# Kernel tuning notes

Measured on AMD Instinct MI355X. Metric: run time of the kernel, lower is better.

Reference implementation:

```python
import jax, jax.numpy as jnp
import numpy as np

NUM_CLASSES = 21
OVERLAP_THRESH = 0.5
POS_PRIOR_THRESH = 0.01
NEGPOS_RATIO = 3
ARM_VAR = (0.1, 0.2)
VAR = (0.1, 0.2)
B, P, NOBJ = 64, 16320, 32


def _iou(a, b):
    # a: [N,4] point-form, b: [P,4] point-form -> [N,P]
    lt = jnp.maximum(a[:, None, :2], b[None, :, :2])
    rb = jnp.minimum(a[:, None, 2:], b[None, :, 2:])
    wh = jnp.clip(rb - lt, 0.0)
    inter = wh[..., 0] * wh[..., 1]
    area_a = (a[:, 2] - a[:, 0]) * (a[:, 3] - a[:, 1])
    area_b = (b[:, 2] - b[:, 0]) * (b[:, 3] - b[:, 1])
    return inter / (area_a[:, None] + area_b[None, :] - inter)


def _decode_point(loc, priors, var):
    # loc: [P,4], priors: [P,4] center-form -> [P,4] point-form
    cxcy = priors[:, :2] + loc[:, :2] * var[0] * priors[:, 2:]
    wh = priors[:, 2:] * jnp.exp(loc[:, 2:] * var[1])
    return jnp.concatenate([cxcy - wh / 2, cxcy + wh / 2], axis=-1)


def _encode(matched, priors, var):
    # matched: [P,4] point-form gt, priors: [P,4] center-form -> [P,4]
    g_cxcy = ((matched[:, :2] + matched[:, 2:]) / 2 - priors[:, :2]) / (var[0] * priors[:, 2:])
    g_wh = jnp.log((matched[:, 2:] - matched[:, :2]) / priors[:, 2:]) / var[1]
    return jnp.concatenate([g_cxcy, g_wh], axis=-1)


def _match_one(truths, labels, dec_point, ref_center, reserve):
    # truths:[N,4] labels:[N] dec_point/ref_center:[P,4] reserve:[P] bool
    n_obj = truths.shape[0]
    ov = _iou(truths, dec_point)                       # [N,P]
    ovm = jnp.where(reserve[None, :], ov, -1.0)        # mask out filtered priors
    best_prior_idx = jnp.argmax(ovm, axis=1)           # [N]
    best_truth_overlap = jnp.max(ovm, axis=0)          # [P]
    best_truth_idx = jnp.argmax(ovm, axis=0)           # [P]
    best_truth_overlap = best_truth_overlap.at[best_prior_idx].set(2.0)
    best_truth_idx = best_truth_idx.at[best_prior_idx].set(jnp.arange(n_obj))
    matched = truths[best_truth_idx]                   # [P,4]
    conf = labels[best_truth_idx] + 1                  # [P]
    conf = jnp.where(best_truth_overlap < OVERLAP_THRESH, 0, conf)
    loc = _encode(matched, ref_center, VAR)
    conf = jnp.where(reserve, conf, -1)                # ignored priors
    loc = jnp.where(reserve[:, None], loc, 0.0)
    return loc, conf


def setup_inputs() -> dict:
    key = jax.random.key(0)
    ks = jax.random.split(key, 8)
    arm_loc = 0.1 * jax.random.normal(ks[0], (B, P, 4), dtype=jnp.float32)
    arm_conf = jax.random.normal(ks[1], (B, P, 2), dtype=jnp.float32)
    odm_loc = jax.random.normal(ks[2], (B, P, 4), dtype=jnp.float32)
    odm_conf = jax.random.normal(ks[3], (B, P, NUM_CLASSES), dtype=jnp.float32)
    # center-form anchors: valid cx,cy,w,h
    cxcy = jax.random.uniform(ks[4], (P, 2), minval=0.02, maxval=0.98)
    wh = jax.random.uniform(ks[5], (P, 2), minval=0.05, maxval=0.4)
    priors = jnp.concatenate([cxcy, wh], axis=-1).astype(jnp.float32)
    # valid point-form ground-truth boxes
    tc = jax.random.uniform(ks[6], (B, NOBJ, 2), minval=0.2, maxval=0.8)
    tw = jax.random.uniform(ks[7], (B, NOBJ, 2), minval=0.05, maxval=0.3)
    truths = jnp.concatenate([tc - tw / 2, tc + tw / 2], axis=-1).astype(jnp.float32)
    labels = jax.random.randint(jax.random.fold_in(key, 9), (B, NOBJ), 0, 20)
    return {"arm_loc": arm_loc, "arm_conf": arm_conf, "odm_loc": odm_loc,
            "odm_conf": odm_conf, "priors": priors, "truths": truths,
            "labels": labels}


def reference(arm_loc, arm_conf, odm_loc, odm_conf, priors, truths, labels):
    # ARM branch and targets are constants w.r.t. gradients (torch uses .data)
    arm_loc = jax.lax.stop_gradient(arm_loc)
    arm_conf = jax.lax.stop_gradient(arm_conf)
    truths = jax.lax.stop_gradient(truths)
    priors = jax.lax.stop_gradient(priors)

    arm_pos_prob = jax.nn.softmax(arm_conf, axis=-1)[..., 1]       # [B,P]
    reserve = arm_pos_prob > POS_PRIOR_THRESH                      # [B,P]
    dec_point = jax.vmap(lambda l: _decode_point(l, priors, ARM_VAR))(arm_loc)  # [B,P,4]
    ref_center = jnp.concatenate([(dec_point[..., :2] + dec_point[..., 2:]) / 2,
                                  dec_point[..., 2:] - dec_point[..., :2]], axis=-1)
    loc_t, conf_t = jax.vmap(_match_one)(truths, labels, dec_point, ref_center, reserve)
    loc_t = jax.lax.stop_gradient(loc_t)
    conf_t = jax.lax.stop_gradient(conf_t)

    pos = conf_t > 0                                               # [B,P]
    ignore = conf_t == -1
    conf_t0 = jnp.where(ignore, 0, conf_t)

    # localization: smooth L1 over positives (sum)
    d = jnp.abs(odm_loc - loc_t)
    sl1 = jnp.where(d < 1.0, 0.5 * d * d, d - 0.5)
    loss_l = jnp.sum(sl1 * pos[..., None].astype(sl1.dtype))

    # per-prior CE: logsumexp - target logit
    lse = jax.nn.logsumexp(odm_conf, axis=-1)                      # [B,P]
    tgt = jnp.take_along_axis(odm_conf, conf_t0[..., None], axis=-1)[..., 0]
    ce = lse - tgt                                                 # [B,P]

    # hard-negative mining: rank negatives by CE (double argsort)
    mine = jnp.where(pos | ignore, 0.0, ce)
    order = jnp.argsort(-mine, axis=1)
    rank = jnp.argsort(order, axis=1)
    num_pos = jnp.sum(pos, axis=1, keepdims=True)                  # [B,1]
    num_neg = jnp.minimum(NEGPOS_RATIO * num_pos, P - 1)
    neg = rank < num_neg

    loss_c = jnp.sum(jnp.where(pos | neg, ce, 0.0))
    total_num = jnp.sum(num_pos).astype(jnp.float32)
    return (loss_l / total_num, loss_c / total_num)
```

## Files before the change

### kernel.cpp

```cpp
#include <hip/hip_runtime.h>

#define B 64
#define P 16320
#define NOBJ 32
#define NC 21
#define CHUNK 4080

__device__ constexpr float LN99 = 4.59511985013459f;
#define SENT 0x407FFFFFFFFFFFFFULL

__global__ void k_init(int* num_pos, float* ll_b, float* lc_b) {
    int t = threadIdx.x;
    if (t < B) { num_pos[t] = 0; ll_b[t] = 0.f; lc_b[t] = 0.f; }
}

__global__ __launch_bounds__(1024) void k_p1(
    const float* __restrict__ arm_loc, const float* __restrict__ arm_conf,
    const float* __restrict__ priors, const float* __restrict__ truths,
    int* __restrict__ bt_pack, unsigned long long* __restrict__ bp_part)
{
    int b = blockIdx.x >> 2, c = blockIdx.x & 3;
    int tid = threadIdx.x;
    int base = c * CHUNK;

    __shared__ float4 s_tr[NOBJ];
    __shared__ float s_ta[NOBJ];
    __shared__ unsigned long long s1[NOBJ * 256];
    __shared__ unsigned long long s2[1024];

    if (tid < NOBJ) {
        float4 t = ((const float4*)truths)[b * NOBJ + tid];
        s_tr[tid] = t;
        s_ta[tid] = (t.z - t.x) * (t.w - t.y);
    }
    __syncthreads();

    float x1[4], y1[4], x2[4], y2[4], ap[4];
    bool rs[4], av[4];
    #pragma unroll
    for (int g = 0; g < 4; g++) {
        int off = g * 1024 + tid;
        av[g] = off < CHUNK;
        rs[g] = false;
        x1[g] = y1[g] = x2[g] = y2[g] = ap[g] = 0.f;
        if (av[g]) {
            int p = base + off;
            size_t bpi = (size_t)b * P + p;
            float2 cc = ((const float2*)arm_conf)[bpi];
            rs[g] = (cc.x - cc.y) < LN99;
            float4 l = ((const float4*)arm_loc)[bpi];
            float4 pr = ((const float4*)priors)[p];
            float dcx = pr.x + l.x * 0.1f * pr.z;
            float dcy = pr.y + l.y * 0.1f * pr.w;
            float dw = pr.z * __expf(l.z * 0.2f);
            float dh = pr.w * __expf(l.w * 0.2f);
            x1[g] = dcx - dw * 0.5f; y1[g] = dcy - dh * 0.5f;
            x2[g] = dcx + dw * 0.5f; y2[g] = dcy + dh * 0.5f;
            ap[g] = (x2[g] - x1[g]) * (y2[g] - y1[g]);
        }
    }

    float bv[4] = {-1.f, -1.f, -1.f, -1.f};
    int bj[4] = {0, 0, 0, 0};

    #pragma unroll
    for (int j = 0; j < NOBJ; j++) {
        float4 t = s_tr[j];
        float ta = s_ta[j];
        float jv = -1.f; int jg = 0;
        #pragma unroll
        for (int g = 0; g < 4; g++) {
            float iw = fmaxf(fminf(x2[g], t.z) - fmaxf(x1[g], t.x), 0.f);
            float ih = fmaxf(fminf(y2[g], t.w) - fmaxf(y1[g], t.y), 0.f);
            float inter = iw * ih;
            float iou = inter * __builtin_amdgcn_rcpf(ta + ap[g] - inter);
            float iou_r = av[g] ? iou : -1.f;
            if (iou_r > bv[g]) { bv[g] = iou_r; bj[g] = j; }
            float iou_m = rs[g] ? iou_r : -1.f;
            if (iou_m > jv) { jv = iou_m; jg = g; }
        }
        unsigned long long pk = 0ULL;
        if (jv >= 0.f) {
            unsigned p = (unsigned)(base + jg * 1024 + tid);
            pk = ((unsigned long long)(__float_as_uint(jv) | 0x80000000u) << 32)
               | (unsigned)~p;
        }
        { unsigned long long o = __shfl_xor(pk, 1, 64); if (o > pk) pk = o; }
        { unsigned long long o = __shfl_xor(pk, 2, 64); if (o > pk) pk = o; }
        if ((tid & 3) == 0) s1[j * 256 + (tid >> 2)] = pk;
    }

    #pragma unroll
    for (int g = 0; g < 4; g++) {
        if (av[g]) {
            int p = base + g * 1024 + tid;
            int bt = rs[g] ? ((bj[g] << 2) | ((bv[g] >= 0.5f) ? 2 : 0) | 1) : 0;
            bt_pack[(size_t)b * P + p] = bt;
        }
    }
    __syncthreads();

    {
        int j = tid >> 5, r = tid & 31;
        unsigned long long m = 0;
        #pragma unroll
        for (int q = 0; q < 8; q++) {
            unsigned long long v = s1[j * 256 + q * 32 + r];
            if (v > m) m = v;
        }
        s2[tid] = m;
    }
    __syncthreads();
    if (tid < NOBJ) {
        unsigned long long m = 0;
        #pragma unroll
        for (int i = 0; i < 32; i++) {
            unsigned long long v = s2[tid * 32 + ((i + tid) & 31)];
            if (v > m) m = v;
        }
        bp_part[blockIdx.x * NOBJ + tid] = m;
    }
}

__global__ __launch_bounds__(256) void k_p2(
    const float* __restrict__ arm_loc, const float* __restrict__ odm_loc,
    const float* __restrict__ odm_conf, const float* __restrict__ priors,
    const float* __restrict__ truths, const int* __restrict__ labels,
    const int* __restrict__ bt_pack, const unsigned long long* __restrict__ bp_part,
    float* __restrict__ mine, int* __restrict__ num_pos,
    float* __restrict__ ll_b, float* __restrict__ lc_b)
{
    int b = blockIdx.y;
    int pbase = blockIdx.x * 256;
    int tid = threadIdx.x;
    int p = pbase + tid;

    __shared__ float soc[256 * NC];
    __shared__ float4 s_tr[NOBJ];
    __shared__ int s_lab[NOBJ];
    __shared__ int s_ov[256];

    s_ov[tid] = -1;
    if (tid < NOBJ) {
        float4 t = ((const float4*)truths)[b * NOBJ + tid];
        s_tr[tid] = t;
        s_lab[tid] = labels[b * NOBJ + tid];
    }
    {
        int nval = P - pbase; if (nval > 256) nval = 256;
        int tot4 = (nval * NC) >> 2;
        const float4* src = (const float4*)(odm_conf + ((size_t)b * P + pbase) * NC);
        float4* dst = (float4*)soc;
        for (int i = tid; i < tot4; i += 256) dst[i] = src[i];
    }
    __syncthreads();

    if (tid < NOBJ) {
        unsigned long long m = SENT;
        #pragma unroll
        for (int c = 0; c < 4; c++) {
            unsigned long long v = bp_part[(b * 4 + c) * NOBJ + tid];
            if (v > m) m = v;
        }
        int pi = (int)~(unsigned)(m & 0xFFFFFFFFULL);
        if (pi >= pbase && pi < pbase + 256) atomicMax(&s_ov[pi - pbase], tid);
    }
    __syncthreads();

    float ll = 0.f, lc = 0.f; int np = 0;
    if (p < P) {
        size_t bpi = (size_t)b * P + p;
        int bt = bt_pack[bpi];
        bool resv = bt & 1;
        int ge = (bt >> 1) & 1;
        int bi = bt >> 2;
        int ov = s_ov[tid];
        if (ov >= 0) { ge = 1; bi = ov; }

        int conf = !resv ? -1 : (ge ? s_lab[bi] + 1 : 0);

        const float* row = &soc[tid * NC];
        float mx = row[0];
        #pragma unroll
        for (int k = 1; k < NC; k++) mx = fmaxf(mx, row[k]);
        float s = 0.f;
        #pragma unroll
        for (int k = 0; k < NC; k++) s += __expf(row[k] - mx);
        int t0 = conf > 0 ? conf : 0;
        float ce = mx + __logf(s) - row[t0];

        mine[bpi] = (conf == 0) ? ce : 0.f;

        if (conf > 0) {
            np = 1; lc = ce;
            float4 l = ((const float4*)arm_loc)[bpi];
            float4 pr = ((const float4*)priors)[p];
            float dcx = pr.x + l.x * 0.1f * pr.z;
            float dcy = pr.y + l.y * 0.1f * pr.w;
            float dw = pr.z * __expf(l.z * 0.2f);
            float dh = pr.w * __expf(l.w * 0.2f);
            float rx1 = dcx - dw * 0.5f, ry1 = dcy - dh * 0.5f;
            float rx2 = dcx + dw * 0.5f, ry2 = dcy + dh * 0.5f;
            float rcx = (rx1 + rx2) * 0.5f, rcy = (ry1 + ry2) * 0.5f;
            float rw = rx2 - rx1, rh = ry2 - ry1;
            float4 tb = s_tr[bi];
            float g0 = ((tb.x + tb.z) * 0.5f - rcx) * __builtin_amdgcn_rcpf(0.1f * rw);
            float g1 = ((tb.y + tb.w) * 0.5f - rcy) * __builtin_amdgcn_rcpf(0.1f * rh);
            float g2 = __logf((tb.z - tb.x) * __builtin_amdgcn_rcpf(rw)) * 5.0f;
            float g3 = __logf((tb.w - tb.y) * __builtin_amdgcn_rcpf(rh)) * 5.0f;
            float4 ol = ((const float4*)odm_loc)[bpi];
            float gt[4] = {g0, g1, g2, g3};
            float od[4] = {ol.x, ol.y, ol.z, ol.w};
            #pragma unroll
            for (int k = 0; k < 4; k++) {
                float d = fabsf(od[k] - gt[k]);
                ll += (d < 1.f) ? 0.5f * d * d : d - 0.5f;
            }
        }
    }

    #pragma unroll
    for (int off = 32; off; off >>= 1) {
        ll += __shfl_xor(ll, off, 64);
        lc += __shfl_xor(lc, off, 64);
        np += __shfl_xor(np, off, 64);
    }
    __shared__ float sll[4], slc[4];
    __shared__ int snp[4];
    int wid = tid >> 6, lane = tid & 63;
    if (lane == 0) { sll[wid] = ll; slc[wid] = lc; snp[wid] = np; }
    __syncthreads();
    if (tid == 0) {
        float a = 0.f, cq = 0.f; int n = 0;
        for (int w = 0; w < 4; w++) { a += sll[w]; cq += slc[w]; n += snp[w]; }
        if (a != 0.f) atomicAdd(&ll_b[b], a);
        if (cq != 0.f) atomicAdd(&lc_b[b], cq);
        if (n) atomicAdd(&num_pos[b], n);
    }
}

__global__ __launch_bounds__(1024) void k_select(
    const float* __restrict__ mine, const int* __restrict__ num_pos,
    float* __restrict__ lc_b)
{
    int b = blockIdx.x, tid = threadIdx.x;
    int K0 = num_pos[b] * 3;
    if (K0 > P - 1) K0 = P - 1;
    if (K0 <= 0) return;

    __shared__ float4 s_row4[P / 4];
    __shared__ unsigned hist[16 * 257];
    __shared__ unsigned s_merged[256];
    __shared__ unsigned s_beta, s_K;
    __shared__ float sS[16];
    __shared__ unsigned sM[16];

    const float4* src = (const float4*)(mine + (size_t)b * P);
    for (int i = tid; i < P / 4; i += 1024) s_row4[i] = src[i];

    unsigned K = (unsigned)K0, prefix = 0, maskDone = 0;
    int wid = tid >> 6;

    for (int pass = 0; pass < 4; pass++) {
        int shift = 24 - pass * 8;
        for (int i = tid; i < 16 * 257; i += 1024) hist[i] = 0;
        __syncthreads();
        for (int i = tid; i < P / 4; i += 1024) {
            float4 v = s_row4[i];
            float vv[4] = {v.x, v.y, v.z, v.w};
            #pragma unroll
            for (int e = 0; e < 4; e++) {
                unsigned bits = __float_as_uint(vv[e]);
                if ((bits & maskDone) == prefix)
                    atomicAdd(&hist[wid * 257 + ((bits >> shift) & 255u)], 1u);
            }
        }
        __syncthreads();
        if (tid < 256) {
            unsigned t = 0;
            #pragma unroll
            for (int w = 0; w < 16; w++) t += hist[w * 257 + tid];
            s_merged[tid] = t;
        }
        __syncthreads();
        if (tid < 64) {
            unsigned u0 = s_merged[tid * 4 + 0], u1 = s_merged[tid * 4 + 1];
            unsigned u2 = s_merged[tid * 4 + 2], u3 = s_merged[tid * 4 + 3];
            unsigned sum4 = u0 + u1 + u2 + u3;
            unsigned x = sum4;
            #pragma unroll
            for (int off = 1; off < 64; off <<= 1) {
                unsigned y = __shfl_down(x, off, 64);
                if (tid + off < 64) x += y;
            }
            unsigned sf0 = x, sf1 = x - u0, sf2 = x - u0 - u1, sf3 = x - u0 - u1 - u2;
            unsigned sf4 = x - sum4;
            if (sf0 >= K && sf1 < K) { s_beta = tid * 4 + 0; s_K = K - sf1; }
            if (sf1 >= K && sf2 < K) { s_beta = tid * 4 + 1; s_K = K - sf2; }
            if (sf2 >= K && sf3 < K) { s_beta = tid * 4 + 2; s_K = K - sf3; }
            if (sf3 >= K && sf4 < K) { s_beta = tid * 4 + 3; s_K = K - sf4; }
        }
        __syncthreads();
        prefix |= (s_beta << shift);
        maskDone |= (0xFFu << shift);
        K = s_K;
        __syncthreads();
    }

    unsigned tBits = prefix;
    float t = __uint_as_float(tBits);

    unsigned mcnt = 0; float ssum = 0.f;
    for (int i = tid; i < P / 4; i += 1024) {
        float4 v = s_row4[i];
        float vv[4] = {v.x, v.y, v.z, v.w};
        #pragma unroll
        for (int e = 0; e < 4; e++) {
            if (__float_as_uint(vv[e]) > tBits) { mcnt++; ssum += vv[e]; }
        }
    }
    #pragma unroll
    for (int off = 32; off; off >>= 1) {
        mcnt += __shfl_xor(mcnt, off, 64);
        ssum += __shfl_xor(ssum, off, 64);
    }
    int lane = tid & 63;
    if (lane == 0) { sS[wid] = ssum; sM[wid] = mcnt; }
    __syncthreads();
    if (tid == 0) {
        float S = 0.f; unsigned M = 0;
        for (int w = 0; w < 16; w++) { S += sS[w]; M += sM[w]; }
        atomicAdd(&lc_b[b], S + (float)(K0 - (int)M) * t);
    }
}

__global__ void k_final(const int* __restrict__ num_pos, const float* __restrict__ ll_b,
                        const float* __restrict__ lc_b, float* __restrict__ out) {
    int t = threadIdx.x;
    int np = num_pos[t];
    float ll = ll_b[t];
    float lc = lc_b[t];
    #pragma unroll
    for (int off = 32; off; off >>= 1) {
        np += __shfl_xor(np, off, 64);
        ll += __shfl_xor(ll, off, 64);
        lc += __shfl_xor(lc, off, 64);
    }
    if (t == 0) {
        float tn = (float)np;
        out[0] = ll / tn;
        out[1] = lc / tn;
    }
}

extern "C" void kernel_launch(void* const* d_in, const int* in_sizes, int n_in,
                              void* d_out, int out_size, void* d_ws, size_t ws_size,
                              hipStream_t stream) {
    const float* arm_loc  = (const float*)d_in[0];
    const float* arm_conf = (const float*)d_in[1];
    const float* odm_loc  = (const float*)d_in[2];
    const float* odm_conf = (const float*)d_in[3];
    const float* priors   = (const float*)d_in[4];
    const float* truths   = (const float*)d_in[5];
    const int*   labels   = (const int*)d_in[6];
    float* out = (float*)d_out;

    char* ws = (char*)d_ws;
    const size_t BPTOT = (size_t)B * P;
    float* mine    = (float*)ws;
    int*   bt_pack = (int*)(ws + 4ull * BPTOT);
    unsigned long long* bp_part = (unsigned long long*)(ws + 8ull * BPTOT);
    int*   num_pos = (int*)(ws + 8ull * BPTOT + 65536ull);
    float* ll_b    = (float*)(ws + 8ull * BPTOT + 65536ull + 256ull);
    float* lc_b    = (float*)(ws + 8ull * BPTOT + 65536ull + 512ull);

    k_init<<<1, 64, 0, stream>>>(num_pos, ll_b, lc_b);
    k_p1<<<256, 1024, 0, stream>>>(arm_loc, arm_conf, priors, truths,
                                   bt_pack, bp_part);
    k_p2<<<dim3(64, B), 256, 0, stream>>>(arm_loc, odm_loc, odm_conf, priors,
                                          truths, labels, bt_pack, bp_part,
                                          mine, num_pos, ll_b, lc_b);
    k_select<<<B, 1024, 0, stream>>>(mine, num_pos, lc_b);
    k_final<<<1, 64, 0, stream>>>(num_pos, ll_b, lc_b, out);
}
```

Measured before the change: 248.9 us.

## Fuse matching and loss passes into one kernel with per-truth correction pass

```diff
diff --git a/kernel.cpp b/kernel.cpp
--- a/kernel.cpp
+++ b/kernel.cpp
@@ -4,218 +4,136 @@
 #define P 16320
 #define NOBJ 32
 #define NC 21
-#define CHUNK 4080
+#define TPB 512
+#define NCH 32
 
 __device__ constexpr float LN99 = 4.59511985013459f;
 #define SENT 0x407FFFFFFFFFFFFFULL
 
-__global__ void k_init(int* num_pos, float* ll_b, float* lc_b) {
-    int t = threadIdx.x;
-    if (t < B) { num_pos[t] = 0; ll_b[t] = 0.f; lc_b[t] = 0.f; }
-}
-
-__global__ __launch_bounds__(1024) void k_p1(
+struct Box { float x1, y1, x2, y2, area; };
+
+__device__ __forceinline__ Box decode_box(float4 l, float4 pr) {
+    Box b;
+    float dcx = pr.x + l.x * 0.1f * pr.z;
+    float dcy = pr.y + l.y * 0.1f * pr.w;
+    float dw = pr.z * __expf(l.z * 0.2f);
+    float dh = pr.w * __expf(l.w * 0.2f);
+    b.x1 = dcx - dw * 0.5f; b.y1 = dcy - dh * 0.5f;
+    b.x2 = dcx + dw * 0.5f; b.y2 = dcy + dh * 0.5f;
+    b.area = (b.x2 - b.x1) * (b.y2 - b.y1);
+    return b;
+}
+__device__ __forceinline__ float iou_box(const Box& bb, float4 t, float ta) {
+    float iw = fmaxf(fminf(bb.x2, t.z) - fmaxf(bb.x1, t.x), 0.f);
+    float ih = fmaxf(fminf(bb.y2, t.w) - fmaxf(bb.y1, t.y), 0.f);
+    float inter = iw * ih;
+    return inter * __builtin_amdgcn_rcpf(ta + bb.area - inter);
+}
+__device__ __forceinline__ float smoothl1(const Box& bb, float4 tb, float4 ol) {
+    float rcx = (bb.x1 + bb.x2) * 0.5f, rcy = (bb.y1 + bb.y2) * 0.5f;
+    float rw = bb.x2 - bb.x1, rh = bb.y2 - bb.y1;
+    float g0 = ((tb.x + tb.z) * 0.5f - rcx) * __builtin_amdgcn_rcpf(0.1f * rw);
+    float g1 = ((tb.y + tb.w) * 0.5f - rcy) * __builtin_amdgcn_rcpf(0.1f * rh);
+    float g2 = __logf((tb.z - tb.x) * __builtin_amdgcn_rcpf(rw)) * 5.0f;
+    float g3 = __logf((tb.w - tb.y) * __builtin_amdgcn_rcpf(rh)) * 5.0f;
+    float gt[4] = {g0, g1, g2, g3};
+    float od[4] = {ol.x, ol.y, ol.z, ol.w};
+    float s = 0.f;
+    #pragma unroll
+    for (int k = 0; k < 4; k++) {
+        float d = fabsf(od[k] - gt[k]);
+        s += (d < 1.f) ? 0.5f * d * d : d - 0.5f;
+    }
+    return s;
+}
+__device__ __forceinline__ float lse_row(const float* row) {
+    float m = row[0];
+    #pragma unroll
+    for (int k = 1; k < NC; k++) m = fmaxf(m, row[k]);
+    float s = 0.f;
+    #pragma unroll
+    for (int k = 0; k < NC; k++) s += __expf(row[k] - m);
+    return m + __logf(s);
+}
+
+__global__ __launch_bounds__(TPB) void k_main(
     const float* __restrict__ arm_loc, const float* __restrict__ arm_conf,
+    const float* __restrict__ odm_loc, const float* __restrict__ odm_conf,
     const float* __restrict__ priors, const float* __restrict__ truths,
-    int* __restrict__ bt_pack, unsigned long long* __restrict__ bp_part)
+    const int* __restrict__ labels,
+    float* __restrict__ mine, unsigned long long* __restrict__ bp_part,
+    float* __restrict__ pll, float* __restrict__ plc, int* __restrict__ pnp)
 {
-    int b = blockIdx.x >> 2, c = blockIdx.x & 3;
+    int b = blockIdx.y, ch = blockIdx.x;
     int tid = threadIdx.x;
-    int base = c * CHUNK;
-
+    int pbase = ch * TPB;
+    int p = pbase + tid;
+    bool active = p < P;
+
+    __shared__ float soc[TPB * NC];
     __shared__ float4 s_tr[NOBJ];
     __shared__ float s_ta[NOBJ];
-    __shared__ unsigned long long s1[NOBJ * 256];
-    __shared__ unsigned long long s2[1024];
+    __shared__ int s_lab[NOBJ];
+    __shared__ unsigned long long s_bp[NOBJ];
+    __shared__ float sll[TPB / 64], slc[TPB / 64];
+    __shared__ int snp[TPB / 64];
 
     if (tid < NOBJ) {
         float4 t = ((const float4*)truths)[b * NOBJ + tid];
         s_tr[tid] = t;
         s_ta[tid] = (t.z - t.x) * (t.w - t.y);
-    }
-    __syncthreads();
-
-    float x1[4], y1[4], x2[4], y2[4], ap[4];
-    bool rs[4], av[4];
-    #pragma unroll
-    for (int g = 0; g < 4; g++) {
-        int off = g * 1024 + tid;
-        av[g] = off < CHUNK;
-        rs[g] = false;
-        x1[g] = y1[g] = x2[g] = y2[g] = ap[g] = 0.f;
-        if (av[g]) {
-            int p = base + off;
-            size_t bpi = (size_t)b * P + p;
-            float2 cc = ((const float2*)arm_conf)[bpi];
-            rs[g] = (cc.x - cc.y) < LN99;
-            float4 l = ((const float4*)arm_loc)[bpi];
-            float4 pr = ((const float4*)priors)[p];
-            float dcx = pr.x + l.x * 0.1f * pr.z;
-            float dcy = pr.y + l.y * 0.1f * pr.w;
-            float dw = pr.z * __expf(l.z * 0.2f);
-            float dh = pr.w * __expf(l.w * 0.2f);
-            x1[g] = dcx - dw * 0.5f; y1[g] = dcy - dh * 0.5f;
-            x2[g] = dcx + dw * 0.5f; y2[g] = dcy + dh * 0.5f;
-            ap[g] = (x2[g] - x1[g]) * (y2[g] - y1[g]);
-        }
-    }
-
-    float bv[4] = {-1.f, -1.f, -1.f, -1.f};
-    int bj[4] = {0, 0, 0, 0};
-
-    #pragma unroll
-    for (int j = 0; j < NOBJ; j++) {
-        float4 t = s_tr[j];
-        float ta = s_ta[j];
-        float jv = -1.f; int jg = 0;
-        #pragma unroll
-        for (int g = 0; g < 4; g++) {
-            float iw = fmaxf(fminf(x2[g], t.z) - fmaxf(x1[g], t.x), 0.f);
-            float ih = fmaxf(fminf(y2[g], t.w) - fmaxf(y1[g], t.y), 0.f);
-            float inter = iw * ih;
-            float iou = inter * __builtin_amdgcn_rcpf(ta + ap[g] - inter);
-            float iou_r = av[g] ? iou : -1.f;
-            if (iou_r > bv[g]) { bv[g] = iou_r; bj[g] = j; }
-            float iou_m = rs[g] ? iou_r : -1.f;
-            if (iou_m > jv) { jv = iou_m; jg = g; }
-        }
-        unsigned long long pk = 0ULL;
-        if (jv >= 0.f) {
-            unsigned p = (unsigned)(base + jg * 1024 + tid);
-            pk = ((unsigned long long)(__float_as_uint(jv) | 0x80000000u) << 32)
-               | (unsigned)~p;
-        }
-        { unsigned long long o = __shfl_xor(pk, 1, 64); if (o > pk) pk = o; }
-        { unsigned long long o = __shfl_xor(pk, 2, 64); if (o > pk) pk = o; }
-        if ((tid & 3) == 0) s1[j * 256 + (tid >> 2)] = pk;
-    }
-
-    #pragma unroll
-    for (int g = 0; g < 4; g++) {
-        if (av[g]) {
-            int p = base + g * 1024 + tid;
-            int bt = rs[g] ? ((bj[g] << 2) | ((bv[g] >= 0.5f) ? 2 : 0) | 1) : 0;
-            bt_pack[(size_t)b * P + p] = bt;
-        }
-    }
-    __syncthreads();
-
+        s_lab[tid] = labels[b * NOBJ + tid];
+        s_bp[tid] = 0ULL;
+    }
     {
-        int j = tid >> 5, r = tid & 31;
-        unsigned long long m = 0;
-        #pragma unroll
-        for (int q = 0; q < 8; q++) {
-            unsigned long long v = s1[j * 256 + q * 32 + r];
-            if (v > m) m = v;
-        }
-        s2[tid] = m;
-    }
-    __syncthreads();
-    if (tid < NOBJ) {
-        unsigned long long m = 0;
-        #pragma unroll
-        for (int i = 0; i < 32; i++) {
-            unsigned long long v = s2[tid * 32 + ((i + tid) & 31)];
-            if (v > m) m = v;
-        }
-        bp_part[blockIdx.x * NOBJ + tid] = m;
-    }
-}
-
-__global__ __launch_bounds__(256) void k_p2(
-    const float* __restrict__ arm_loc, const float* __restrict__ odm_loc,
-    const float* __restrict__ odm_conf, const float* __restrict__ priors,
-    const float* __restrict__ truths, const int* __restrict__ labels,
-    const int* __restrict__ bt_pack, const unsigned long long* __restrict__ bp_part,
-    float* __restrict__ mine, int* __restrict__ num_pos,
-    float* __restrict__ ll_b, float* __restrict__ lc_b)
-{
-    int b = blockIdx.y;
-    int pbase = blockIdx.x * 256;
-    int tid = threadIdx.x;
-    int p = pbase + tid;
-
-    __shared__ float soc[256 * NC];
-    __shared__ float4 s_tr[NOBJ];
-    __shared__ int s_lab[NOBJ];
-    __shared__ int s_ov[256];
-
-    s_ov[tid] = -1;
-    if (tid < NOBJ) {
-        float4 t = ((const float4*)truths)[b * NOBJ + tid];
-        s_tr[tid] = t;
-        s_lab[tid] = labels[b * NOBJ + tid];
-    }
-    {
-        int nval = P - pbase; if (nval > 256) nval = 256;
+        int nval = P - pbase; if (nval > TPB) nval = TPB;
         int tot4 = (nval * NC) >> 2;
         const float4* src = (const float4*)(odm_conf + ((size_t)b * P + pbase) * NC);
         float4* dst = (float4*)soc;
-        for (int i = tid; i < tot4; i += 256) dst[i] = src[i];
+        for (int i = tid; i < tot4; i += TPB) dst[i] = src[i];
     }
     __syncthreads();
 
-    if (tid < NOBJ) {
-        unsigned long long m = SENT;
-        #pragma unroll
-        for (int c = 0; c < 4; c++) {
-            unsigned long long v = bp_part[(b * 4 + c) * NOBJ + tid];
-            if (v > m) m = v;
-        }
-        int pi = (int)~(unsigned)(m & 0xFFFFFFFFULL);
-        if (pi >= pbase && pi < pbase + 256) atomicMax(&s_ov[pi - pbase], tid);
-    }
-    __syncthreads();
+    Box bb = {0.f, 0.f, 0.f, 0.f, 0.f};
+    bool resv = false;
+    if (active) {
+        size_t bpi = (size_t)b * P + p;
+        float2 cc = ((const float2*)arm_conf)[bpi];
+        resv = (cc.x - cc.y) < LN99;
+        bb = decode_box(((const float4*)arm_loc)[bpi], ((const float4*)priors)[p]);
+    }
+
+    float bv = -1.f; int bj = 0;
+    volatile unsigned* bp_hi = (volatile unsigned*)s_bp;
+    #pragma unroll
+    for (int j = 0; j < NOBJ; j++) {
+        float iou = iou_box(bb, s_tr[j], s_ta[j]);
+        if (iou > bv) { bv = iou; bj = j; }
+        if (resv) {
+            unsigned hv = __float_as_uint(iou) | 0x80000000u;
+            if (hv >= bp_hi[2 * j + 1]) {
+                unsigned long long key =
+                    ((unsigned long long)hv << 32) | (unsigned)~(unsigned)p;
+                atomicMax(&s_bp[j], key);
+            }
+        }
+    }
+
+    int conf = -1;
+    if (active) conf = resv ? ((bv >= 0.5f) ? s_lab[bj] + 1 : 0) : -1;
 
     float ll = 0.f, lc = 0.f; int np = 0;
-    if (p < P) {
+    if (active) {
         size_t bpi = (size_t)b * P + p;
-        int bt = bt_pack[bpi];
-        bool resv = bt & 1;
-        int ge = (bt >> 1) & 1;
-        int bi = bt >> 2;
-        int ov = s_ov[tid];
-        if (ov >= 0) { ge = 1; bi = ov; }
-
-        int conf = !resv ? -1 : (ge ? s_lab[bi] + 1 : 0);
-
         const float* row = &soc[tid * NC];
-        float mx = row[0];
-        #pragma unroll
-        for (int k = 1; k < NC; k++) mx = fmaxf(mx, row[k]);
-        float s = 0.f;
-        #pragma unroll
-        for (int k = 0; k < NC; k++) s += __expf(row[k] - mx);
+        float lse = lse_row(row);
         int t0 = conf > 0 ? conf : 0;
-        float ce = mx + __logf(s) - row[t0];
-
+        float ce = lse - row[t0];
         mine[bpi] = (conf == 0) ? ce : 0.f;
-
         if (conf > 0) {
             np = 1; lc = ce;
-            float4 l = ((const float4*)arm_loc)[bpi];
-            float4 pr = ((const float4*)priors)[p];
-            float dcx = pr.x + l.x * 0.1f * pr.z;
-            float dcy = pr.y + l.y * 0.1f * pr.w;
-            float dw = pr.z * __expf(l.z * 0.2f);
-            float dh = pr.w * __expf(l.w * 0.2f);
-            float rx1 = dcx - dw * 0.5f, ry1 = dcy - dh * 0.5f;
-            float rx2 = dcx + dw * 0.5f, ry2 = dcy + dh * 0.5f;
-            float rcx = (rx1 + rx2) * 0.5f, rcy = (ry1 + ry2) * 0.5f;
-            float rw = rx2 - rx1, rh = ry2 - ry1;
-            float4 tb = s_tr[bi];
-            float g0 = ((tb.x + tb.z) * 0.5f - rcx) * __builtin_amdgcn_rcpf(0.1f * rw);
-            float g1 = ((tb.y + tb.w) * 0.5f - rcy) * __builtin_amdgcn_rcpf(0.1f * rh);
-            float g2 = __logf((tb.z - tb.x) * __builtin_amdgcn_rcpf(rw)) * 5.0f;
-            float g3 = __logf((tb.w - tb.y) * __builtin_amdgcn_rcpf(rh)) * 5.0f;
             float4 ol = ((const float4*)odm_loc)[bpi];
-            float gt[4] = {g0, g1, g2, g3};
-            float od[4] = {ol.x, ol.y, ol.z, ol.w};
-            #pragma unroll
-            for (int k = 0; k < 4; k++) {
-                float d = fabsf(od[k] - gt[k]);
-                ll += (d < 1.f) ? 0.5f * d * d : d - 0.5f;
-            }
+            ll = smoothl1(bb, s_tr[bj], ol);
         }
     }
 
@@ -225,18 +143,106 @@
         lc += __shfl_xor(lc, off, 64);
         np += __shfl_xor(np, off, 64);
     }
-    __shared__ float sll[4], slc[4];
-    __shared__ int snp[4];
     int wid = tid >> 6, lane = tid & 63;
     if (lane == 0) { sll[wid] = ll; slc[wid] = lc; snp[wid] = np; }
     __syncthreads();
+
+    if (tid < NOBJ) bp_part[((size_t)b * NCH + ch) * NOBJ + tid] = s_bp[tid];
     if (tid == 0) {
-        float a = 0.f, cq = 0.f; int n = 0;
-        for (int w = 0; w < 4; w++) { a += sll[w]; cq += slc[w]; n += snp[w]; }
-        if (a != 0.f) atomicAdd(&ll_b[b], a);
-        if (cq != 0.f) atomicAdd(&lc_b[b], cq);
-        if (n) atomicAdd(&num_pos[b], n);
-    }
+        float a = 0.f, c = 0.f; int n = 0;
+        #pragma unroll
+        for (int w = 0; w < TPB / 64; w++) { a += sll[w]; c += slc[w]; n += snp[w]; }
+        int idx = b * NCH + ch;
+        pll[idx] = a; plc[idx] = c; pnp[idx] = n;
+    }
+}
+
+__global__ __launch_bounds__(64) void k_fix(
+    const float* __restrict__ arm_loc, const float* __restrict__ arm_conf,
+    const float* __restrict__ odm_loc, const float* __restrict__ odm_conf,
+    const float* __restrict__ priors, const float* __restrict__ truths,
+    const int* __restrict__ labels,
+    const unsigned long long* __restrict__ bp_part,
+    const float* __restrict__ pll, const float* __restrict__ plc,
+    const int* __restrict__ pnp,
+    float* __restrict__ mine, float* __restrict__ ll_b, float* __restrict__ lc_b,
+    int* __restrict__ num_pos)
+{
+    int b = blockIdx.x;
+    int tid = threadIdx.x;
+
+    __shared__ float4 s_tr[NOBJ];
+    __shared__ float s_ta[NOBJ];
+    __shared__ int s_lab[NOBJ];
+    __shared__ unsigned s_p[NOBJ];
+
+    if (tid < NOBJ) {
+        float4 t = ((const float4*)truths)[b * NOBJ + tid];
+        s_tr[tid] = t;
+        s_ta[tid] = (t.z - t.x) * (t.w - t.y);
+        s_lab[tid] = labels[b * NOBJ + tid];
+    }
+
+    float ll = 0.f, lc = 0.f; int np = 0;
+    if (tid < NCH) {
+        int idx = b * NCH + tid;
+        ll = pll[idx]; lc = plc[idx]; np = pnp[idx];
+    }
+
+    if (tid < NOBJ) {
+        unsigned long long m = SENT;
+        for (int c = 0; c < NCH; c++) {
+            unsigned long long v = bp_part[((size_t)b * NCH + c) * NOBJ + tid];
+            if (v > m) m = v;
+        }
+        s_p[tid] = ~(unsigned)(m & 0xFFFFFFFFULL);
+    }
+
+    if (tid < NOBJ) {
+        unsigned pstar = s_p[tid];
+        bool alive = true;
+        for (int j2 = tid + 1; j2 < NOBJ; j2++)
+            if (s_p[j2] == pstar) alive = false;
+        if (alive) {
+            size_t bpi = (size_t)b * P + pstar;
+            float2 cc = ((const float2*)arm_conf)[bpi];
+            bool resv = (cc.x - cc.y) < LN99;
+            if (resv) {
+                Box bb = decode_box(((const float4*)arm_loc)[bpi],
+                                    ((const float4*)priors)[pstar]);
+                float bv = -1.f; int bj = 0;
+                #pragma unroll
+                for (int j = 0; j < NOBJ; j++) {
+                    float iou = iou_box(bb, s_tr[j], s_ta[j]);
+                    if (iou > bv) { bv = iou; bj = j; }
+                }
+                int old_conf = (bv >= 0.5f) ? s_lab[bj] + 1 : 0;
+                const float* row = odm_conf + bpi * NC;
+                float lse = lse_row(row);
+                int new_conf = s_lab[tid] + 1;
+                float ce_new = lse - row[new_conf];
+                float4 ol = ((const float4*)odm_loc)[bpi];
+                float sl_new = smoothl1(bb, s_tr[tid], ol);
+                if (old_conf > 0) {
+                    float ce_old = lse - row[old_conf];
+                    float sl_old = smoothl1(bb, s_tr[bj], ol);
+                    lc += ce_new - ce_old;
+                    ll += sl_new - sl_old;
+                } else {
+                    lc += ce_new; ll += sl_new; np += 1;
+                    mine[bpi] = 0.f;
+                }
+            }
+        }
+    }
+
+    #pragma unroll
+    for (int off = 32; off; off >>= 1) {
+        ll += __shfl_xor(ll, off, 64);
+        lc += __shfl_xor(lc, off, 64);
+        np += __shfl_xor(np, off, 64);
+    }
+    if (tid == 0) { ll_b[b] = ll; lc_b[b] = lc; num_pos[b] = np; }
 }
 
 __global__ __launch_bounds__(1024) void k_select(
@@ -315,9 +321,8 @@
         float4 v = s_row4[i];
         float vv[4] = {v.x, v.y, v.z, v.w};
         #pragma unroll
-        for (int e = 0; e < 4; e++) {
+        for (int e = 0; e < 4; e++)
             if (__float_as_uint(vv[e]) > tBits) { mcnt++; ssum += vv[e]; }
-        }
     }
     #pragma unroll
     for (int off = 32; off; off >>= 1) {
@@ -330,7 +335,7 @@
     if (tid == 0) {
         float S = 0.f; unsigned M = 0;
         for (int w = 0; w < 16; w++) { S += sS[w]; M += sM[w]; }
-        atomicAdd(&lc_b[b], S + (float)(K0 - (int)M) * t);
+        lc_b[b] += S + (float)(K0 - (int)M) * t;
     }
 }
 
@@ -367,19 +372,23 @@
 
     char* ws = (char*)d_ws;
     const size_t BPTOT = (size_t)B * P;
-    float* mine    = (float*)ws;
-    int*   bt_pack = (int*)(ws + 4ull * BPTOT);
-    unsigned long long* bp_part = (unsigned long long*)(ws + 8ull * BPTOT);
-    int*   num_pos = (int*)(ws + 8ull * BPTOT + 65536ull);
-    float* ll_b    = (float*)(ws + 8ull * BPTOT + 65536ull + 256ull);
-    float* lc_b    = (float*)(ws + 8ull * BPTOT + 65536ull + 512ull);
-
-    k_init<<<1, 64, 0, stream>>>(num_pos, ll_b, lc_b);
-    k_p1<<<256, 1024, 0, stream>>>(arm_loc, arm_conf, priors, truths,
-                                   bt_pack, bp_part);
-    k_p2<<<dim3(64, B), 256, 0, stream>>>(arm_loc, odm_loc, odm_conf, priors,
-                                          truths, labels, bt_pack, bp_part,
-                                          mine, num_pos, ll_b, lc_b);
+    float* mine = (float*)ws;
+    unsigned long long* bp_part = (unsigned long long*)(ws + 4ull * BPTOT);
+    char* ws2 = ws + 4ull * BPTOT + 8ull * B * NCH * NOBJ;
+    float* pll = (float*)ws2;
+    float* plc = (float*)(ws2 + 4ull * B * NCH);
+    int*   pnp = (int*)(ws2 + 8ull * B * NCH);
+    char* ws3 = ws2 + 12ull * B * NCH;
+    float* ll_b = (float*)ws3;
+    float* lc_b = (float*)(ws3 + 4 * B);
+    int* num_pos = (int*)(ws3 + 8 * B);
+
+    k_main<<<dim3(NCH, B), TPB, 0, stream>>>(arm_loc, arm_conf, odm_loc, odm_conf,
+                                             priors, truths, labels,
+                                             mine, bp_part, pll, plc, pnp);
+    k_fix<<<B, 64, 0, stream>>>(arm_loc, arm_conf, odm_loc, odm_conf, priors,
+                                truths, labels, bp_part, pll, plc, pnp,
+                                mine, ll_b, lc_b, num_pos);
     k_select<<<B, 1024, 0, stream>>>(mine, num_pos, lc_b);
     k_final<<<1, 64, 0, stream>>>(num_pos, ll_b, lc_b, out);
 }
```

Result: slower. 604.9 us (+143.0%).
